# Performance work log

Hardware: AMD Instinct MI355X
Metric: run time of the kernel (lower is better)

## Reference

```python
import jax, jax.numpy as jnp
import numpy as np

B, C, H, W = 8, 512, 32, 32
NUM_HEADS = 8
HEAD_DIM = C // NUM_HEADS
SCALE = 1.0 / float(np.sqrt(HEAD_DIM))


def setup_inputs() -> dict:
    key = jax.random.key(0)
    ks = jax.random.split(key, 6)
    x = jax.random.normal(ks[0], (B, C, H, W), dtype=jnp.float32)
    attn_mask = jax.random.randint(ks[1], (B, H, W), 0, 2).astype(jnp.bool_)
    # 1x1 conv weights are equivalent to channel matmuls: (out_ch, in_ch)
    w_std = 1.0 / float(np.sqrt(C))
    qkv_w = jax.random.uniform(ks[2], (3 * C, C), jnp.float32, -w_std, w_std)
    qkv_b = jax.random.uniform(ks[3], (3 * C,), jnp.float32, -w_std, w_std)
    proj_w = jax.random.uniform(ks[4], (C, C), jnp.float32, -w_std, w_std)
    proj_b = jax.random.uniform(ks[5], (C,), jnp.float32, -w_std, w_std)
    return {"x": x, "attn_mask": attn_mask, "qkv_w": qkv_w, "qkv_b": qkv_b,
            "proj_w": proj_w, "proj_b": proj_b}


def reference(x, attn_mask, qkv_w, qkv_b, proj_w, proj_b):
    b, c, h, w = x.shape
    S = h * w
    neg = jnp.finfo(x.dtype).min
    # qkv 1x1 conv: (B,3C,H,W)
    qkv = jnp.einsum('oc,bchw->bohw', qkv_w, x) + qkv_b[None, :, None, None]
    q, k, v = jnp.split(qkv, 3, axis=1)

    def split_heads(z):
        # (B, C, H, W) -> (B, heads, head_dim, S)
        return z.reshape(b, NUM_HEADS, HEAD_DIM, S)

    q, k, v = split_heads(q), split_heads(k), split_heads(v)
    # scores[s,t] = sum_d q[d,s] * k[d,t]
    scores = jnp.einsum('bhds,bhdt->bhst', q, k) * SCALE
    idx = jnp.arange(S)
    causal = (idx[None, :] > idx[:, None])[None, None]  # (1,1,S,S), True above diag
    scores = jnp.where(causal, neg, scores)
    kpm = attn_mask.reshape(b, 1, 1, S)  # key padding mask, True = mask out
    scores = jnp.where(kpm, neg, scores)
    attn = jax.nn.softmax(scores, axis=-1)
    # ctx[d,s] = sum_t v[d,t] * attn[s,t]
    ctx = jnp.einsum('bhdt,bhst->bhds', v, attn)
    ctx = ctx.reshape(b, c, h, w)
    out = jnp.einsum('oc,bchw->bohw', proj_w, ctx) + proj_b[None, :, None, None]
    return out
```

## Files before the change

### kernel.cpp

```cpp
#include <hip/hip_runtime.h>
#include <cfloat>
#include <math.h>

#define SB 1024
#define CC 512
#define NB 8
#define NH 8
#define HD 64

typedef short short8 __attribute__((ext_vector_type(8)));
typedef short s16x4 __attribute__((ext_vector_type(4)));
typedef float f32x4 __attribute__((ext_vector_type(4)));

__device__ __forceinline__ short f2bs(float f) {
    union { float f; unsigned u; } x; x.f = f;
    unsigned r = x.u + 0x7fffu + ((x.u >> 16) & 1u);
    return (short)(r >> 16);
}

__device__ __forceinline__ void gload16(const void* g, void* l) {
    __builtin_amdgcn_global_load_lds(
        (const __attribute__((address_space(1))) unsigned int*)g,
        (__attribute__((address_space(3))) unsigned int*)l, 16, 0, 0);
}

__device__ __forceinline__ int sidx(int row, int colb) {
    return row * 64 + ((colb ^ ((row & 7) << 4)) >> 1);
}

__global__ __launch_bounds__(256)
void prep(const float* __restrict__ w1, const float* __restrict__ w2,
          short* __restrict__ o1, short* __restrict__ o2,
          const float* __restrict__ x, short* __restrict__ xT,
          const int* __restrict__ mask, float* __restrict__ maskf,
          float* __restrict__ vmean)
{
    const int B = blockIdx.x;
    const int tid = threadIdx.x;
    if (B < 1024) {
        const int i4 = B * 256 + tid;
        const int N1 = 1536 * 512 / 4;
        if (i4 < N1) {
            float4 v = *(const float4*)&w1[(size_t)i4 * 4];
            s16x4 p; p[0] = f2bs(v.x); p[1] = f2bs(v.y); p[2] = f2bs(v.z); p[3] = f2bs(v.w);
            *(s16x4*)&o1[(size_t)i4 * 4] = p;
        } else {
            const int j = i4 - N1;
            float4 v = *(const float4*)&w2[(size_t)j * 4];
            s16x4 p; p[0] = f2bs(v.x); p[1] = f2bs(v.y); p[2] = f2bs(v.z); p[3] = f2bs(v.w);
            *(s16x4*)&o2[(size_t)j * 4] = p;
        }
    } else if (B < 2048) {
        const int idx = B - 1024;
        const int bs = idx & 15, bc = (idx >> 4) & 7, b = idx >> 7;
        __shared__ short T[64][72];
        {
            const int cl = tid >> 4;
            const int s4 = (tid & 15) * 4;
            #pragma unroll
            for (int r = 0; r < 4; ++r) {
                const int c = cl + 16 * r;
                float4 v = *(const float4*)&x[((size_t)b * CC + bc * 64 + c) * SB + bs * 64 + s4];
                T[s4 + 0][c] = f2bs(v.x); T[s4 + 1][c] = f2bs(v.y);
                T[s4 + 2][c] = f2bs(v.z); T[s4 + 3][c] = f2bs(v.w);
            }
        }
        __syncthreads();
        {
            const int sl = tid >> 2;
            const int c16 = (tid & 3) * 16;
            short8 v0 = *(const short8*)&T[sl][c16];
            short8 v1 = *(const short8*)&T[sl][c16 + 8];
            short* dst = &xT[((size_t)b * SB + bs * 64 + sl) * CC + bc * 64 + c16];
            *(short8*)&dst[0] = v0;
            *(short8*)&dst[8] = v1;
        }
    } else if (B < 2080) {
        const int gi = (B - 2048) * 256 + tid;
        if (gi < NB * SB) maskf[gi] = (mask[gi] != 0) ? -FLT_MAX : 0.f;
    } else {
        const int i = (B - 2080) * 256 + tid;
        if (i < NB * CC) vmean[i] = 0.f;
    }
}

template<int MODE>
__global__ __launch_bounds__(256)
void gemm_bf16(const short* __restrict__ A, const float* __restrict__ bias,
               const short* __restrict__ BT,
               short* __restrict__ qTo, short* __restrict__ kTo,
               short* __restrict__ vo, float* __restrict__ fo,
               float* __restrict__ vmean)
{
    const int stile = blockIdx.x * 128;
    const int bo    = blockIdx.y;
    const int b     = blockIdx.z;
    const int tid   = threadIdx.x;
    const int wave = tid >> 6, lane = tid & 63, lg = lane >> 4, ln = lane & 15;
    const int wm = wave >> 1, wn = wave & 1;

    __shared__ short Al[128 * 64];
    __shared__ short Bl[128 * 64];

    f32x4 acc[4][4];
    #pragma unroll
    for (int mt = 0; mt < 4; ++mt)
        #pragma unroll
        for (int nt = 0; nt < 4; ++nt) acc[mt][nt] = (f32x4){0.f, 0.f, 0.f, 0.f};

    const char* Ab = (const char*)(A + (size_t)bo * 128 * 512);
    const char* Bb = (const char*)(BT + ((size_t)b * SB + stile) * 512);

    for (int kc = 0; kc < 512; kc += 64) {
        __syncthreads();
        #pragma unroll
        for (int sw = 0; sw < 4; ++sw) {
            const int lin = tid * 16 + sw * 4096;
            const int row = lin >> 7;
            const int scol = (lin & 127) ^ ((row & 7) << 4);
            gload16(Ab + ((size_t)row * 512 + kc) * 2 + scol,
                    (char*)Al + (wave << 10) + (sw << 12));
            gload16(Bb + ((size_t)row * 512 + kc) * 2 + scol,
                    (char*)Bl + (wave << 10) + (sw << 12));
        }
        __syncthreads();
        #pragma unroll
        for (int kk = 0; kk < 2; ++kk) {
            const int colb = kk * 64 + lg * 16;
            short8 a[4], bb[4];
            #pragma unroll
            for (int mt = 0; mt < 4; ++mt)
                a[mt] = *(const short8*)&Al[sidx(wm * 64 + mt * 16 + ln, colb)];
            #pragma unroll
            for (int nt = 0; nt < 4; ++nt)
                bb[nt] = *(const short8*)&Bl[sidx(wn * 64 + nt * 16 + ln, colb)];
            #pragma unroll
            for (int mt = 0; mt < 4; ++mt)
                #pragma unroll
                for (int nt = 0; nt < 4; ++nt)
                    acc[mt][nt] = __builtin_amdgcn_mfma_f32_16x16x32_bf16(
                        a[mt], bb[nt], acc[mt][nt], 0, 0, 0);
        }
    }

    const int s_base = stile + wn * 64;
    if (MODE == 0) {
        if (bo < 8) {
            short* dst = (bo < 4) ? qTo : kTo;
            const int h = (bo & 3) * 2 + wm;
            const float sc = (bo < 4) ? 0.18033688011112042f : 1.0f;
            #pragma unroll
            for (int mt = 0; mt < 4; ++mt) {
                const int d0 = mt * 16 + 4 * lg;
                const int o0 = bo * 128 + wm * 64 + d0;
                const float b0 = bias[o0], b1 = bias[o0 + 1],
                            b2 = bias[o0 + 2], b3 = bias[o0 + 3];
                #pragma unroll
                for (int nt = 0; nt < 4; ++nt) {
                    const int s = s_base + nt * 16 + ln;
                    s16x4 pk;
                    pk[0] = f2bs((acc[mt][nt][0] + b0) * sc);
                    pk[1] = f2bs((acc[mt][nt][1] + b1) * sc);
                    pk[2] = f2bs((acc[mt][nt][2] + b2) * sc);
                    pk[3] = f2bs((acc[mt][nt][3] + b3) * sc);
                    *(s16x4*)&dst[(((size_t)b * NH + h) * SB + s) * HD + d0] = pk;
                }
            }
        } else {
            #pragma unroll
            for (int mt = 0; mt < 4; ++mt) {
                const int cv0 = (bo - 8) * 128 + wm * 64 + mt * 16 + 4 * lg;
                #pragma unroll
                for (int r = 0; r < 4; ++r) {
                    const float bv = bias[1024 + cv0 + r];
                    float part = 0.f;
                    #pragma unroll
                    for (int nt = 0; nt < 4; ++nt) {
                        const int s = s_base + nt * 16 + ln;
                        const float val = acc[mt][nt][r] + bv;
                        part += val;
                        vo[((size_t)b * CC + cv0 + r) * SB + s] = f2bs(val);
                    }
                    #pragma unroll
                    for (int o = 1; o < 16; o <<= 1)
                        part += __shfl_xor(part, o, 64);
                    if (ln == 0)
                        atomicAdd(&vmean[(size_t)b * CC + cv0 + r], part);
                }
            }
        }
    } else {
        #pragma unroll
        for (int mt = 0; mt < 4; ++mt) {
            #pragma unroll
            for (int r = 0; r < 4; ++r) {
                const int o = bo * 128 + wm * 64 + mt * 16 + 4 * lg + r;
                const float bv = bias[o];
                #pragma unroll
                for (int nt = 0; nt < 4; ++nt) {
                    const int s = s_base + nt * 16 + ln;
                    fo[((size_t)b * CC + o) * SB + s] = acc[mt][nt][r] + bv;
                }
            }
        }
    }
}

__global__ __launch_bounds__(512, 4)
void attn_mfma(const short* __restrict__ qT, const short* __restrict__ kT,
               const short* __restrict__ vN, const float* __restrict__ maskf,
               const float* __restrict__ vmean, short* __restrict__ ctxT)
{
    const int L  = blockIdx.x;
    const int p  = 7 - (L >> 6);
    const int bh = L & 63;
    const int b  = bh >> 3, h = bh & 7;
    const int tid = threadIdx.x;
    const int wave = tid >> 6;
    const int lane = tid & 63;
    const int lg = lane >> 4;
    const int ln = lane & 15;

    const int qbm  = 2 * p + (wave >> 2);
    const int wsub = wave & 3;
    const int tend = 2 * p + 1;

    __shared__ short Ks[2][64 * 64];
    __shared__ short Vs[2][64 * 64];
    __shared__ float mskL[2][64];
    __shared__ short Ps[8][16][72];

    const char*  kbh = (const char*)(kT + (((size_t)b * NH + h) * SB) * HD);
    const char*  vbh = (const char*)(vN + ((size_t)b * CC + h * HD) * SB);
    const float* mb  = maskf + (size_t)b * SB;

    short8 qa0, qa1;
    {
        const short* qrow = qT + (((size_t)b * NH + h) * SB + qbm * 64 + wsub * 16 + ln) * HD;
        qa0 = *(const short8*)&qrow[8 * lg];
        qa1 = *(const short8*)&qrow[32 + 8 * lg];
    }

    float m_ = -FLT_MAX, l_ = 0.f;
    f32x4 acc[4];
    #pragma unroll
    for (int nt = 0; nt < 4; ++nt) acc[nt] = (f32x4){0.f, 0.f, 0.f, 0.f};

    auto stage = [&](int tb, int bi) {
        const int lin = tid * 16;
        const int row = lin >> 7;
        const int scol = (lin & 127) ^ ((row & 7) << 4);
        gload16(kbh + (size_t)tb * 128 + row * 128 + scol,
                (char*)&Ks[bi][0] + (wave << 10));
        gload16(vbh + (size_t)row * (SB * 2) + tb * 2 + scol,
                (char*)&Vs[bi][0] + (wave << 10));
        if (tid < 64) mskL[bi][tid] = mb[tb + tid];
    };

    int cur = 0;
    stage(0, 0);
    __syncthreads();

    for (int t = 0; t <= tend; ++t) {
        if (t < tend) stage((t + 1) * 64, cur ^ 1);
        const bool mine = (t <= qbm);

        if (mine) {
            f32x4 sc[4];
            #pragma unroll
            for (int nt = 0; nt < 4; ++nt) {
                short8 kb0 = *(const short8*)&Ks[cur][sidx(ln + 16 * nt, lg * 16)];
                short8 kb1 = *(const short8*)&Ks[cur][sidx(ln + 16 * nt, 64 + lg * 16)];
                f32x4 z = (f32x4){0.f, 0.f, 0.f, 0.f};
                z = __builtin_amdgcn_mfma_f32_16x16x32_bf16(kb0, qa0, z, 0, 0, 0);
                z = __builtin_amdgcn_mfma_f32_16x16x32_bf16(kb1, qa1, z, 0, 0, 0);
                sc[nt] = z;
            }

            #pragma unroll
            for (int nt = 0; nt < 4; ++nt) {
                const float4 mf = *(const float4*)&mskL[cur][16 * nt + 4 * lg];
                sc[nt][0] += mf.x; sc[nt][1] += mf.y;
                sc[nt][2] += mf.z; sc[nt][3] += mf.w;
            }
            if (t == qbm) {
                const int so = wsub * 16 + ln;
                #pragma unroll
                for (int nt = 0; nt < 4; ++nt)
                    #pragma unroll
                    for (int r = 0; r < 4; ++r)
                        if (16 * nt + 4 * lg + r > so) sc[nt][r] = -FLT_MAX;
            }

            float mx = sc[0][0];
            #pragma unroll
            for (int nt = 0; nt < 4; ++nt)
                #pragma unroll
                for (int r = 0; r < 4; ++r)
                    if (nt | r) mx = fmaxf(mx, sc[nt][r]);
            mx = fmaxf(mx, __shfl_xor(mx, 16, 64));
            mx = fmaxf(mx, __shfl_xor(mx, 32, 64));

            if (!__all(mx <= m_ + 11.5f)) {
                const float mnew = fmaxf(m_, mx);
                const float fq = exp2f(m_ - mnew);
                l_ *= fq;
                #pragma unroll
                for (int nt = 0; nt < 4; ++nt)
                    #pragma unroll
                    for (int r = 0; r < 4; ++r) acc[nt][r] *= fq;
                m_ = mnew;
            }

            float rs = 0.f;
            #pragma unroll
            for (int nt = 0; nt < 4; ++nt) {
                s16x4 pk;
                #pragma unroll
                for (int r = 0; r < 4; ++r) {
                    const float pv = exp2f(sc[nt][r] - m_);
                    rs += pv;
                    pk[r] = f2bs(pv);
                }
                *(s16x4*)&Ps[wave][ln][16 * nt + 4 * lg] = pk;
            }
            rs += __shfl_xor(rs, 16, 64);
            rs += __shfl_xor(rs, 32, 64);
            l_ += rs;

            const short8 pa0 = *(const short8*)&Ps[wave][ln][8 * lg];
            const short8 pa1 = *(const short8*)&Ps[wave][ln][32 + 8 * lg];
            #pragma unroll
            for (int nt = 0; nt < 4; ++nt) {
                short8 va0 = *(const short8*)&Vs[cur][sidx(16 * nt + ln, lg * 16)];
                short8 va1 = *(const short8*)&Vs[cur][sidx(16 * nt + ln, 64 + lg * 16)];
                acc[nt] = __builtin_amdgcn_mfma_f32_16x16x32_bf16(va0, pa0, acc[nt], 0, 0, 0);
                acc[nt] = __builtin_amdgcn_mfma_f32_16x16x32_bf16(va1, pa1, acc[nt], 0, 0, 0);
            }
        }

        if (t < tend) {
            __syncthreads();
            cur ^= 1;
        }
    }

    const float rl = 1.f / l_;
    const bool dead = (m_ == -FLT_MAX);
    const float* vmb = vmean + (size_t)b * CC + h * HD;
    const int s = qbm * 64 + wsub * 16 + ln;
    short* crow = ctxT + ((size_t)b * SB + s) * CC + h * HD;
    #pragma unroll
    for (int nt = 0; nt < 4; ++nt) {
        const int d0 = 16 * nt + 4 * lg;
        const float4 vm4 = *(const float4*)&vmb[d0];
        s16x4 pk;
        pk[0] = f2bs(dead ? vm4.x * (1.f / 1024.f) : acc[nt][0] * rl);
        pk[1] = f2bs(dead ? vm4.y * (1.f / 1024.f) : acc[nt][1] * rl);
        pk[2] = f2bs(dead ? vm4.z * (1.f / 1024.f) : acc[nt][2] * rl);
        pk[3] = f2bs(dead ? vm4.w * (1.f / 1024.f) : acc[nt][3] * rl);
        *(s16x4*)&crow[d0] = pk;
    }
}

extern "C" void kernel_launch(void* const* d_in, const int* in_sizes, int n_in,
                              void* d_out, int out_size, void* d_ws, size_t ws_size,
                              hipStream_t stream) {
    const float* x      = (const float*)d_in[0];
    const int*   amask  = (const int*)d_in[1];
    const float* qkv_w  = (const float*)d_in[2];
    const float* qkv_b  = (const float*)d_in[3];
    const float* proj_w = (const float*)d_in[4];
    const float* proj_b = (const float*)d_in[5];
    float* out = (float*)d_out;

    short* xT    = (short*)d_ws;
    short* w1b   = xT  + (size_t)NB * SB * CC;
    short* w2b   = w1b + (size_t)1536 * 512;
    short* qT    = w2b + (size_t)512 * 512;
    short* kT    = qT  + (size_t)NB * NH * SB * HD;
    short* vN    = kT  + (size_t)NB * NH * SB * HD;
    short* ctxT  = vN  + (size_t)NB * CC * SB;
    float* vmean = (float*)(ctxT + (size_t)NB * SB * CC);
    float* maskf = vmean + (size_t)NB * CC;

    prep<<<2096, 256, 0, stream>>>(qkv_w, proj_w, w1b, w2b, x, xT,
                                   amask, maskf, vmean);
    gemm_bf16<0><<<dim3(8, 12, NB), 256, 0, stream>>>(
        w1b, qkv_b, xT, qT, kT, vN, nullptr, vmean);
    attn_mfma<<<dim3(512, 1, 1), 512, 0, stream>>>(qT, kT, vN, maskf, vmean, ctxT);
    gemm_bf16<1><<<dim3(8, 4, NB), 256, 0, stream>>>(
        w2b, proj_b, ctxT, nullptr, nullptr, nullptr, out, nullptr);
}
```

Baseline: 89.11 us.

## Split attention blocks to one 64-row query tile per 256-thread block

After: 85.25 us. 1.05x faster.

```diff
diff --git a/kernel.cpp b/kernel.cpp
--- a/kernel.cpp
+++ b/kernel.cpp
@@ -206,13 +206,13 @@
     }
 }
 
-__global__ __launch_bounds__(512, 4)
+__global__ __launch_bounds__(256, 4)
 void attn_mfma(const short* __restrict__ qT, const short* __restrict__ kT,
                const short* __restrict__ vN, const float* __restrict__ maskf,
                const float* __restrict__ vmean, short* __restrict__ ctxT)
 {
     const int L  = blockIdx.x;
-    const int p  = 7 - (L >> 6);
+    const int qb = 15 - (L >> 6);
     const int bh = L & 63;
     const int b  = bh >> 3, h = bh & 7;
     const int tid = threadIdx.x;
@@ -221,14 +221,9 @@
     const int lg = lane >> 4;
     const int ln = lane & 15;
 
-    const int qbm  = 2 * p + (wave >> 2);
-    const int wsub = wave & 3;
-    const int tend = 2 * p + 1;
-
     __shared__ short Ks[2][64 * 64];
     __shared__ short Vs[2][64 * 64];
-    __shared__ float mskL[2][64];
-    __shared__ short Ps[8][16][72];
+    __shared__ short Ps[4][16 * 64];
 
     const char*  kbh = (const char*)(kT + (((size_t)b * NH + h) * SB) * HD);
     const char*  vbh = (const char*)(vN + ((size_t)b * CC + h * HD) * SB);
@@ -236,10 +231,12 @@
 
     short8 qa0, qa1;
     {
-        const short* qrow = qT + (((size_t)b * NH + h) * SB + qbm * 64 + wsub * 16 + ln) * HD;
+        const short* qrow = qT + (((size_t)b * NH + h) * SB + qb * 64 + wave * 16 + ln) * HD;
         qa0 = *(const short8*)&qrow[8 * lg];
         qa1 = *(const short8*)&qrow[32 + 8 * lg];
     }
+
+    const int psw = (ln & 7) << 3;
 
     float m_ = -FLT_MAX, l_ = 0.f;
     f32x4 acc[4];
@@ -247,99 +244,99 @@
     for (int nt = 0; nt < 4; ++nt) acc[nt] = (f32x4){0.f, 0.f, 0.f, 0.f};
 
     auto stage = [&](int tb, int bi) {
-        const int lin = tid * 16;
-        const int row = lin >> 7;
-        const int scol = (lin & 127) ^ ((row & 7) << 4);
-        gload16(kbh + (size_t)tb * 128 + row * 128 + scol,
-                (char*)&Ks[bi][0] + (wave << 10));
-        gload16(vbh + (size_t)row * (SB * 2) + tb * 2 + scol,
-                (char*)&Vs[bi][0] + (wave << 10));
-        if (tid < 64) mskL[bi][tid] = mb[tb + tid];
+        #pragma unroll
+        for (int sw = 0; sw < 2; ++sw) {
+            const int lin = tid * 16 + sw * 4096;
+            const int row = lin >> 7;
+            const int scol = (lin & 127) ^ ((row & 7) << 4);
+            gload16(kbh + (size_t)tb * 128 + row * 128 + scol,
+                    (char*)&Ks[bi][0] + (wave << 10) + (sw << 12));
+            gload16(vbh + (size_t)row * (SB * 2) + tb * 2 + scol,
+                    (char*)&Vs[bi][0] + (wave << 10) + (sw << 12));
+        }
     };
 
     int cur = 0;
     stage(0, 0);
     __syncthreads();
 
-    for (int t = 0; t <= tend; ++t) {
-        if (t < tend) stage((t + 1) * 64, cur ^ 1);
-        const bool mine = (t <= qbm);
-
-        if (mine) {
-            f32x4 sc[4];
-            #pragma unroll
-            for (int nt = 0; nt < 4; ++nt) {
-                short8 kb0 = *(const short8*)&Ks[cur][sidx(ln + 16 * nt, lg * 16)];
-                short8 kb1 = *(const short8*)&Ks[cur][sidx(ln + 16 * nt, 64 + lg * 16)];
-                f32x4 z = (f32x4){0.f, 0.f, 0.f, 0.f};
-                z = __builtin_amdgcn_mfma_f32_16x16x32_bf16(kb0, qa0, z, 0, 0, 0);
-                z = __builtin_amdgcn_mfma_f32_16x16x32_bf16(kb1, qa1, z, 0, 0, 0);
-                sc[nt] = z;
-            }
-
-            #pragma unroll
-            for (int nt = 0; nt < 4; ++nt) {
-                const float4 mf = *(const float4*)&mskL[cur][16 * nt + 4 * lg];
-                sc[nt][0] += mf.x; sc[nt][1] += mf.y;
-                sc[nt][2] += mf.z; sc[nt][3] += mf.w;
-            }
-            if (t == qbm) {
-                const int so = wsub * 16 + ln;
-                #pragma unroll
-                for (int nt = 0; nt < 4; ++nt)
-                    #pragma unroll
-                    for (int r = 0; r < 4; ++r)
-                        if (16 * nt + 4 * lg + r > so) sc[nt][r] = -FLT_MAX;
-            }
-
-            float mx = sc[0][0];
+    for (int t = 0; t <= qb; ++t) {
+        if (t < qb) stage((t + 1) * 64, cur ^ 1);
+
+        f32x4 sc[4];
+        #pragma unroll
+        for (int nt = 0; nt < 4; ++nt) {
+            short8 kb0 = *(const short8*)&Ks[cur][sidx(ln + 16 * nt, lg * 16)];
+            short8 kb1 = *(const short8*)&Ks[cur][sidx(ln + 16 * nt, 64 + lg * 16)];
+            f32x4 z = (f32x4){0.f, 0.f, 0.f, 0.f};
+            z = __builtin_amdgcn_mfma_f32_16x16x32_bf16(kb0, qa0, z, 0, 0, 0);
+            z = __builtin_amdgcn_mfma_f32_16x16x32_bf16(kb1, qa1, z, 0, 0, 0);
+            sc[nt] = z;
+        }
+
+        const int tb = t * 64;
+        #pragma unroll
+        for (int nt = 0; nt < 4; ++nt) {
+            const float4 mf = *(const float4*)&mb[tb + 16 * nt + 4 * lg];
+            sc[nt][0] += mf.x; sc[nt][1] += mf.y;
+            sc[nt][2] += mf.z; sc[nt][3] += mf.w;
+        }
+        if (t == qb) {
+            const int so = wave * 16 + ln;
             #pragma unroll
             for (int nt = 0; nt < 4; ++nt)
                 #pragma unroll
                 for (int r = 0; r < 4; ++r)
-                    if (nt | r) mx = fmaxf(mx, sc[nt][r]);
-            mx = fmaxf(mx, __shfl_xor(mx, 16, 64));
-            mx = fmaxf(mx, __shfl_xor(mx, 32, 64));
-
-            if (!__all(mx <= m_ + 11.5f)) {
-                const float mnew = fmaxf(m_, mx);
-                const float fq = exp2f(m_ - mnew);
-                l_ *= fq;
-                #pragma unroll
-                for (int nt = 0; nt < 4; ++nt)
-                    #pragma unroll
-                    for (int r = 0; r < 4; ++r) acc[nt][r] *= fq;
-                m_ = mnew;
-            }
-
-            float rs = 0.f;
-            #pragma unroll
-            for (int nt = 0; nt < 4; ++nt) {
-                s16x4 pk;
-                #pragma unroll
-                for (int r = 0; r < 4; ++r) {
-                    const float pv = exp2f(sc[nt][r] - m_);
-                    rs += pv;
-                    pk[r] = f2bs(pv);
-                }
-                *(s16x4*)&Ps[wave][ln][16 * nt + 4 * lg] = pk;
-            }
-            rs += __shfl_xor(rs, 16, 64);
-            rs += __shfl_xor(rs, 32, 64);
-            l_ += rs;
-
-            const short8 pa0 = *(const short8*)&Ps[wave][ln][8 * lg];
-            const short8 pa1 = *(const short8*)&Ps[wave][ln][32 + 8 * lg];
-            #pragma unroll
-            for (int nt = 0; nt < 4; ++nt) {
-                short8 va0 = *(const short8*)&Vs[cur][sidx(16 * nt + ln, lg * 16)];
-                short8 va1 = *(const short8*)&Vs[cur][sidx(16 * nt + ln, 64 + lg * 16)];
-                acc[nt] = __builtin_amdgcn_mfma_f32_16x16x32_bf16(va0, pa0, acc[nt], 0, 0, 0);
-                acc[nt] = __builtin_amdgcn_mfma_f32_16x16x32_bf16(va1, pa1, acc[nt], 0, 0, 0);
-            }
-        }
-
-        if (t < tend) {
+                    if (16 * nt + 4 * lg + r > so) sc[nt][r] = -FLT_MAX;
+        }
+
+        float mx = sc[0][0];
+        #pragma unroll
+        for (int nt = 0; nt < 4; ++nt)
+            #pragma unroll
+            for (int r = 0; r < 4; ++r)
+                if (nt | r) mx = fmaxf(mx, sc[nt][r]);
+        mx = fmaxf(mx, __shfl_xor(mx, 16, 64));
+        mx = fmaxf(mx, __shfl_xor(mx, 32, 64));
+
+        if (!__all(mx <= m_ + 11.5f)) {
+            const float mnew = fmaxf(m_, mx);
+            const float fq = exp2f(m_ - mnew);
+            l_ *= fq;
+            #pragma unroll
+            for (int nt = 0; nt < 4; ++nt)
+                #pragma unroll
+                for (int r = 0; r < 4; ++r) acc[nt][r] *= fq;
+            m_ = mnew;
+        }
+
+        float rs = 0.f;
+        #pragma unroll
+        for (int nt = 0; nt < 4; ++nt) {
+            s16x4 pk;
+            #pragma unroll
+            for (int r = 0; r < 4; ++r) {
+                const float p = exp2f(sc[nt][r] - m_);
+                rs += p;
+                pk[r] = f2bs(p);
+            }
+            *(s16x4*)&Ps[wave][ln * 64 + ((16 * nt + 4 * lg) ^ psw)] = pk;
+        }
+        rs += __shfl_xor(rs, 16, 64);
+        rs += __shfl_xor(rs, 32, 64);
+        l_ += rs;
+
+        const short8 pa0 = *(const short8*)&Ps[wave][ln * 64 + ((8 * lg) ^ psw)];
+        const short8 pa1 = *(const short8*)&Ps[wave][ln * 64 + ((32 + 8 * lg) ^ psw)];
+        #pragma unroll
+        for (int nt = 0; nt < 4; ++nt) {
+            short8 va0 = *(const short8*)&Vs[cur][sidx(16 * nt + ln, lg * 16)];
+            short8 va1 = *(const short8*)&Vs[cur][sidx(16 * nt + ln, 64 + lg * 16)];
+            acc[nt] = __builtin_amdgcn_mfma_f32_16x16x32_bf16(va0, pa0, acc[nt], 0, 0, 0);
+            acc[nt] = __builtin_amdgcn_mfma_f32_16x16x32_bf16(va1, pa1, acc[nt], 0, 0, 0);
+        }
+
+        if (t < qb) {
             __syncthreads();
             cur ^= 1;
         }
@@ -348,7 +345,7 @@
     const float rl = 1.f / l_;
     const bool dead = (m_ == -FLT_MAX);
     const float* vmb = vmean + (size_t)b * CC + h * HD;
-    const int s = qbm * 64 + wsub * 16 + ln;
+    const int s = qb * 64 + wave * 16 + ln;
     short* crow = ctxT + ((size_t)b * SB + s) * CC + h * HD;
     #pragma unroll
     for (int nt = 0; nt < 4; ++nt) {
@@ -388,7 +385,7 @@
                                    amask, maskf, vmean);
     gemm_bf16<0><<<dim3(8, 12, NB), 256, 0, stream>>>(
         w1b, qkv_b, xT, qT, kT, vN, nullptr, vmean);
-    attn_mfma<<<dim3(512, 1, 1), 512, 0, stream>>>(qT, kT, vN, maskf, vmean, ctxT);
+    attn_mfma<<<dim3(1024, 1, 1), 256, 0, stream>>>(qT, kT, vN, maskf, vmean, ctxT);
     gemm_bf16<1><<<dim3(8, 4, NB), 256, 0, stream>>>(
         w2b, proj_b, ctxT, nullptr, nullptr, nullptr, out, nullptr);
 }
```
